# Performance work log

Hardware: AMD Instinct MI355X
Metric: run time of the kernel (lower is better)

The kernel has to match this reference:

```python
import jax, jax.numpy as jnp
import numpy as np

HIDDEN = 512
NSTEPS = 100
IN_DIM = 3
OUT_DIM = 3
BATCH = 16384


def _gru_cell(x, h, w_ih, w_hh, b_ih, b_hh):
    # torch.nn.GRUCell math; w_ih: [3H, in], w_hh: [3H, H]
    gi = x @ w_ih.T + b_ih  # [B, 3H]
    gh = h @ w_hh.T + b_hh  # [B, 3H]
    i_r, i_z, i_n = jnp.split(gi, 3, axis=-1)
    h_r, h_z, h_n = jnp.split(gh, 3, axis=-1)
    r = jax.nn.sigmoid(i_r + h_r)
    zt = jax.nn.sigmoid(i_z + h_z)
    n = jnp.tanh(i_n + r * h_n)
    return (1.0 - zt) * n + zt * h


def setup_inputs() -> dict:
    key = jax.random.key(0)
    ks = jax.random.split(key, 12)
    k = 1.0 / np.sqrt(HIDDEN)
    u = lambda kk, shape: jax.random.uniform(kk, shape, jnp.float32, -k, k)
    return {
        "z": jax.random.normal(ks[0], (BATCH, 6), jnp.float32),
        "w_ih1": u(ks[1], (3 * HIDDEN, IN_DIM)),
        "w_hh1": u(ks[2], (3 * HIDDEN, HIDDEN)),
        "b_ih1": u(ks[3], (3 * HIDDEN,)),
        "b_hh1": u(ks[4], (3 * HIDDEN,)),
        "w_ih2": u(ks[5], (3 * HIDDEN, HIDDEN)),
        "w_hh2": u(ks[6], (3 * HIDDEN, HIDDEN)),
        "b_ih2": u(ks[7], (3 * HIDDEN,)),
        "b_hh2": u(ks[8], (3 * HIDDEN,)),
        "fc_w": u(ks[9], (OUT_DIM, HIDDEN)),
        "fc_b": u(ks[10], (OUT_DIM,)),
    }


def reference(z, w_ih1, w_hh1, b_ih1, b_hh1, w_ih2, w_hh2, b_ih2, b_hh2, fc_w, fc_b):
    nbatch = z.shape[0]
    x0 = z[:, 3:]  # [B, 3]
    h1 = jnp.zeros((nbatch, HIDDEN), z.dtype)
    h2 = jnp.zeros((nbatch, HIDDEN), z.dtype)

    def step(carry, _):
        x, h1, h2 = carry
        h1 = _gru_cell(x, h1, w_ih1, w_hh1, b_ih1, b_hh1)
        h2 = _gru_cell(h1, h2, w_ih2, w_hh2, b_ih2, b_hh2)
        x = x + 0.1 * jnp.tanh(h2 @ fc_w.T + fc_b)
        return (x, h1, h2), x

    _, xs = jax.lax.scan(step, (x0, h1, h2), None, length=NSTEPS - 1)
    seq = jnp.concatenate([x0[None], xs], axis=0)  # [T, B, 3]
    return jnp.transpose(seq, (1, 0, 2))  # [B, T, 3]
```

## Files before the change

kernel.cpp:

```cpp
#include <hip/hip_runtime.h>

typedef _Float16 f16;
typedef _Float16 f16x8 __attribute__((ext_vector_type(8)));
typedef float f32x16 __attribute__((ext_vector_type(16)));
typedef unsigned int u32;
typedef u32 u32x2v __attribute__((ext_vector_type(2)));

#define HID   512
#define NSTEP 100

__device__ __forceinline__ f16x8 dec8(u32x2v w) {
  union { u32 u[4]; f16x8 v; } r;
  const u32 a = w[0], b = w[1];
  r.u[0] = ((a & 0x000000ffu) << 8) | ((a & 0x0000ff00u) << 16);
  r.u[1] = ((a >> 8) & 0x0000ff00u) | (a & 0xff000000u);
  r.u[2] = ((b & 0x000000ffu) << 8) | ((b & 0x0000ff00u) << 16);
  r.u[3] = ((b >> 8) & 0x0000ff00u) | (b & 0xff000000u);
  return r.v;
}

__device__ __forceinline__ float sigmoid_f(float x) {
  return 1.0f / (1.0f + __expf(-x));
}
__device__ __forceinline__ float tanh_f(float x) {
  float e = __expf(2.0f * x);
  return 1.0f - 2.0f / (e + 1.0f);
}
__device__ __forceinline__ f32x16 mfma16(f16x8 a, f16x8 b, f32x16 c) {
  return __builtin_amdgcn_mfma_f32_32x32x16_f16(a, b, c, 0, 0, 0);
}
__device__ __forceinline__ f32x16 zero16() {
  f32x16 z;
#pragma unroll
  for (int i = 0; i < 16; ++i) z[i] = 0.f;
  return z;
}

__global__ void pack_wn(const float* __restrict__ W, f16* __restrict__ out) {
  int t = blockIdx.x * 256 + threadIdx.x;
  if (t >= 16 * 32 * 64) return;
  int lane = t & 63;
  int kt   = (t >> 6) & 31;
  int ct   = t >> 11;
  int gate = 1024 + ct * 32 + (lane & 31);
  int k0   = kt * 16 + (lane >> 5) * 8;
  const float* src = W + gate * HID + k0;
  f16x8 v;
#pragma unroll
  for (int i = 0; i < 8; ++i) v[i] = (f16)src[i];
  *(f16x8*)(out + (size_t)t * 8) = v;
}

__global__ void pack_w8(const float* __restrict__ W, unsigned char* __restrict__ out) {
  int t = blockIdx.x * 256 + threadIdx.x;
  if (t >= 2 * 16 * 32 * 64) return;
  int lane = t & 63;
  int kt   = (t >> 6) & 31;
  int ct   = (t >> 11) & 15;
  int g    = t >> 15;
  int gate = g * 512 + ct * 32 + (lane & 31);
  int k0   = kt * 16 + (lane >> 5) * 8;
  const float* src = W + gate * HID + k0;
  unsigned char v[8];
#pragma unroll
  for (int i = 0; i < 8; ++i) {
    f16 h = (f16)src[i];
    unsigned short hb;
    __builtin_memcpy(&hb, &h, 2);
    v[i] = (unsigned char)((hb + 0x80u) >> 8);
  }
  unsigned char* dst = out + (size_t)t * 8;
#pragma unroll
  for (int i = 0; i < 8; ++i) dst[i] = v[i];
}

__global__ void pack_wx(const float* __restrict__ W, const float* __restrict__ bi,
                        const float* __restrict__ bh, f16* __restrict__ out) {
  int t = blockIdx.x * 256 + threadIdx.x;
  if (t >= 48 * 64) return;
  int lane = t & 63;
  int ct   = t >> 6;
  int col  = ct * 32 + (lane & 31);
  int k0   = (lane >> 5) * 8;
  f16x8 v;
#pragma unroll
  for (int i = 0; i < 8; ++i) {
    int k = k0 + i;
    float x = 0.f;
    if (k < 3)       x = W[col * 3 + k];
    else if (k == 3) x = (ct < 32) ? (bi[col] + bh[col]) : bi[col];
    v[i] = (f16)x;
  }
  *(f16x8*)(out + (size_t)t * 8) = v;
}

__global__ void pack_bias(const float* __restrict__ bi, const float* __restrict__ bh,
                          float* __restrict__ out) {
  int j = blockIdx.x * 256 + threadIdx.x;
  if (j < 1024)      out[j] = bi[j] + bh[j];
  else if (j < 1536) out[j] = bi[j];
  else if (j < 2048) out[j] = bh[j - 512];
}

__global__ __launch_bounds__(512, 2) void gru_fused(
    const float* __restrict__ z,
    const float* __restrict__ fc_w,
    const float* __restrict__ fc_b,
    const f16*  __restrict__ Wn,
    const unsigned char* __restrict__ W8,
    const f16*  __restrict__ Wx,
    const float* __restrict__ Bb,
    float* __restrict__ out)
{
  __shared__ f16   h1s[64 * HID];
  __shared__ f16   h2s[64 * HID];
  __shared__ f16   xs16[64 * 16];
  __shared__ float fcwT[3 * HID];
  __shared__ float xsf[64 * 4];
  __shared__ float bsh[5 * 512];

  const int tid  = threadIdx.x;
  const int lane = tid & 63;
  const int wv   = tid >> 6;
  const int b0   = blockIdx.x * 64;

  {
    f16x8 z8 = {0, 0, 0, 0, 0, 0, 0, 0};
    for (int i = tid; i < 64 * HID / 8; i += 512) {
      ((f16x8*)h1s)[i] = z8;
      ((f16x8*)h2s)[i] = z8;
    }
    if (tid < 64) {
#pragma unroll
      for (int k = 0; k < 16; ++k) xs16[tid * 16 + k] = (f16)((k == 3) ? 1.f : 0.f);
    }
    if (tid < HID) {
      const int pos = ((tid & 7) << 6) + (tid >> 3);
      fcwT[pos]        = fc_w[tid];
      fcwT[512 + pos]  = fc_w[512 + tid];
      fcwT[1024 + pos] = fc_w[1024 + tid];
      bsh[tid]         = Bb[1536 + tid];
      bsh[512 + tid]   = Bb[2048 + tid];
      bsh[1024 + tid]  = Bb[2048 + 512 + tid];
      bsh[1536 + tid]  = Bb[2048 + 1024 + tid];
      bsh[2048 + tid]  = Bb[2048 + 1536 + tid];
    }
  }
  __syncthreads();
  if (tid < 64 * 3) {
    const int rr = tid / 3, oo = tid - rr * 3;
    float v = z[(size_t)(b0 + rr) * 6 + 3 + oo];
    xsf[rr * 4 + oo] = v;
    xs16[rr * 16 + oo] = (f16)v;
    out[(size_t)(b0 + rr) * 300 + oo] = v;
  }
  __syncthreads();

  const int colid = lane & 31;
  const int khalf = lane >> 5;
  const int klo   = khalf << 4;
  const int patA  = (colid & 7) << 4;
  const int rbase = colid * 1024;
  const int jw    = wv << 6;
  const int ct0   = wv << 1;
  const int ct1   = ct0 + 1;

  const unsigned char* W8_1r = W8 + (size_t)ct0 * 16384 + lane * 8;
  const unsigned char* W8_1z = W8 + 262144 + (size_t)ct0 * 16384 + lane * 8;
  const unsigned char* W8_ir = W8 + 524288 + (size_t)ct0 * 16384 + lane * 8;
  const unsigned char* W8_iz = W8 + 524288 + 262144 + (size_t)ct0 * 16384 + lane * 8;
  const unsigned char* W8_hr = W8 + 1048576 + (size_t)ct0 * 16384 + lane * 8;
  const unsigned char* W8_hz = W8 + 1048576 + 262144 + (size_t)ct0 * 16384 + lane * 8;
  const f16* Wn_1 = Wn + (size_t)ct0 * 16384 + lane * 8;
  const f16* Wn_i = Wn + 262144 + (size_t)ct0 * 16384 + lane * 8;
  const f16* Wn_h = Wn + 524288 + (size_t)ct0 * 16384 + lane * 8;

  const float fb0 = fc_b[0], fb1 = fc_b[1], fb2 = fc_b[2];
  const int xoff0 = colid * 32 + klo;
  const int xoff1 = (32 + colid) * 32 + klo;

  for (int t = 1; t < NSTEP; ++t) {
    f32x16 aR[2][2], aH[2][2], aZ[2][2];

    {
      f16x8 ax0 = *(const f16x8*)((const char*)xs16 + xoff0);
      f16x8 ax1 = *(const f16x8*)((const char*)xs16 + xoff1);
      f32x16 zz = zero16();
#pragma unroll
      for (int c = 0; c < 2; ++c) {
        f16x8 bx = *(const f16x8*)(Wx + (size_t)(ct0 + c) * 512 + lane * 8);
        aR[c][0] = mfma16(ax0, bx, zz);
        aR[c][1] = mfma16(ax1, bx, zz);
      }
#pragma unroll 2
      for (int kt = 0; kt < 32; ++kt) {
        const int koff = ((kt << 5) | klo) ^ patA;
        f16x8 a0 = *(const f16x8*)((const char*)h1s + rbase + koff);
        f16x8 a1 = *(const f16x8*)((const char*)h1s + 32768 + rbase + koff);
        f16x8 b0 = dec8(*(const u32x2v*)(W8_1r + kt * 512));
        f16x8 b1 = dec8(*(const u32x2v*)(W8_1r + 16384 + kt * 512));
        aR[0][0] = mfma16(a0, b0, aR[0][0]);  aR[0][1] = mfma16(a1, b0, aR[0][1]);
        aR[1][0] = mfma16(a0, b1, aR[1][0]);  aR[1][1] = mfma16(a1, b1, aR[1][1]);
      }
    }
    {
      f32x16 zz = zero16();
      aH[0][0] = zz; aH[0][1] = zz; aH[1][0] = zz; aH[1][1] = zz;
#pragma unroll 2
      for (int kt = 0; kt < 32; ++kt) {
        const int koff = ((kt << 5) | klo) ^ patA;
        f16x8 a0 = *(const f16x8*)((const char*)h1s + rbase + koff);
        f16x8 a1 = *(const f16x8*)((const char*)h1s + 32768 + rbase + koff);
        f16x8 b0 = *(const f16x8*)(Wn_1 + kt * 512);
        f16x8 b1 = *(const f16x8*)(Wn_1 + 16384 + kt * 512);
        aH[0][0] = mfma16(a0, b0, aH[0][0]);  aH[0][1] = mfma16(a1, b0, aH[0][1]);
        aH[1][0] = mfma16(a0, b1, aH[1][0]);  aH[1][1] = mfma16(a1, b1, aH[1][1]);
      }
    }
    {
#pragma unroll
      for (int c = 0; c < 2; ++c) {
        const float bnh = bsh[jw + (c << 5) + colid];
#pragma unroll
        for (int tl = 0; tl < 2; ++tl)
#pragma unroll
          for (int q = 0; q < 16; ++q)
            aH[c][tl][q] = sigmoid_f(aR[c][tl][q]) * (aH[c][tl][q] + bnh);
      }
      f16x8 ax0 = *(const f16x8*)((const char*)xs16 + xoff0);
      f16x8 ax1 = *(const f16x8*)((const char*)xs16 + xoff1);
#pragma unroll
      for (int c = 0; c < 2; ++c) {
        f16x8 bx = *(const f16x8*)(Wx + (size_t)(32 + ct0 + c) * 512 + lane * 8);
        aH[c][0] = mfma16(ax0, bx, aH[c][0]);
        aH[c][1] = mfma16(ax1, bx, aH[c][1]);
      }
    }
    {
      f16x8 ax0 = *(const f16x8*)((const char*)xs16 + xoff0);
      f16x8 ax1 = *(const f16x8*)((const char*)xs16 + xoff1);
      f32x16 zz = zero16();
#pragma unroll
      for (int c = 0; c < 2; ++c) {
        f16x8 bx = *(const f16x8*)(Wx + (size_t)(16 + ct0 + c) * 512 + lane * 8);
        aZ[c][0] = mfma16(ax0, bx, zz);
        aZ[c][1] = mfma16(ax1, bx, zz);
      }
#pragma unroll 2
      for (int kt = 0; kt < 32; ++kt) {
        const int koff = ((kt << 5) | klo) ^ patA;
        f16x8 a0 = *(const f16x8*)((const char*)h1s + rbase + koff);
        f16x8 a1 = *(const f16x8*)((const char*)h1s + 32768 + rbase + koff);
        f16x8 b0 = dec8(*(const u32x2v*)(W8_1z + kt * 512));
        f16x8 b1 = dec8(*(const u32x2v*)(W8_1z + 16384 + kt * 512));
        aZ[0][0] = mfma16(a0, b0, aZ[0][0]);  aZ[0][1] = mfma16(a1, b0, aZ[0][1]);
        aZ[1][0] = mfma16(a0, b1, aZ[1][0]);  aZ[1][1] = mfma16(a1, b1, aZ[1][1]);
      }
    }
    __syncthreads();
#pragma unroll
    for (int c = 0; c < 2; ++c) {
      const int jxc = 2 * (jw + (c << 5) + colid);
#pragma unroll
      for (int tl = 0; tl < 2; ++tl)
#pragma unroll
        for (int q = 0; q < 16; ++q) {
          const int row = (q & 3) + ((q >> 2) << 3) + (khalf << 2);
          f16* hp = (f16*)((char*)h1s + tl * 32768 + row * 1024 + (jxc ^ ((row & 7) << 4)));
          float zt = sigmoid_f(aZ[c][tl][q]);
          float n  = tanh_f(aH[c][tl][q]);
          float hold = (float)*hp;
          *hp = (f16)((1.0f - zt) * n + zt * hold);
        }
    }
    __syncthreads();

    {
      f32x16 zz = zero16();
      aR[0][0] = zz; aR[0][1] = zz; aR[1][0] = zz; aR[1][1] = zz;
#pragma unroll 2
      for (int kt = 0; kt < 32; ++kt) {
        const int koff = ((kt << 5) | klo) ^ patA;
        f16x8 x0 = *(const f16x8*)((const char*)h1s + rbase + koff);
        f16x8 x1 = *(const f16x8*)((const char*)h1s + 32768 + rbase + koff);
        f16x8 y0 = *(const f16x8*)((const char*)h2s + rbase + koff);
        f16x8 y1 = *(const f16x8*)((const char*)h2s + 32768 + rbase + koff);
        f16x8 bi0 = dec8(*(const u32x2v*)(W8_ir + kt * 512));
        f16x8 bi1 = dec8(*(const u32x2v*)(W8_ir + 16384 + kt * 512));
        f16x8 bh0 = dec8(*(const u32x2v*)(W8_hr + kt * 512));
        f16x8 bh1 = dec8(*(const u32x2v*)(W8_hr + 16384 + kt * 512));
        aR[0][0] = mfma16(x0, bi0, aR[0][0]);  aR[0][0] = mfma16(y0, bh0, aR[0][0]);
        aR[0][1] = mfma16(x1, bi0, aR[0][1]);  aR[0][1] = mfma16(y1, bh0, aR[0][1]);
        aR[1][0] = mfma16(x0, bi1, aR[1][0]);  aR[1][0] = mfma16(y0, bh1, aR[1][0]);
        aR[1][1] = mfma16(x1, bi1, aR[1][1]);  aR[1][1] = mfma16(y1, bh1, aR[1][1]);
      }
    }
    {
      f32x16 zz = zero16();
      aH[0][0] = zz; aH[0][1] = zz; aH[1][0] = zz; aH[1][1] = zz;
#pragma unroll 2
      for (int kt = 0; kt < 32; ++kt) {
        const int koff = ((kt << 5) | klo) ^ patA;
        f16x8 y0 = *(const f16x8*)((const char*)h2s + rbase + koff);
        f16x8 y1 = *(const f16x8*)((const char*)h2s + 32768 + rbase + koff);
        f16x8 b0 = *(const f16x8*)(Wn_h + kt * 512);
        f16x8 b1 = *(const f16x8*)(Wn_h + 16384 + kt * 512);
        aH[0][0] = mfma16(y0, b0, aH[0][0]);  aH[0][1] = mfma16(y1, b0, aH[0][1]);
        aH[1][0] = mfma16(y0, b1, aH[1][0]);  aH[1][1] = mfma16(y1, b1, aH[1][1]);
      }
    }
#pragma unroll
    for (int c = 0; c < 2; ++c) {
      const int j = jw + (c << 5) + colid;
      const float br  = bsh[512 + j];
      const float bnh = bsh[2048 + j];
#pragma unroll
      for (int tl = 0; tl < 2; ++tl)
#pragma unroll
        for (int q = 0; q < 16; ++q)
          aH[c][tl][q] = sigmoid_f(aR[c][tl][q] + br) * (aH[c][tl][q] + bnh);
    }
    {
      f32x16 zz = zero16();
      aZ[0][0] = zz; aZ[0][1] = zz; aZ[1][0] = zz; aZ[1][1] = zz;
#pragma unroll 2
      for (int kt = 0; kt < 32; ++kt) {
        const int koff = ((kt << 5) | klo) ^ patA;
        f16x8 x0 = *(const f16x8*)((const char*)h1s + rbase + koff);
        f16x8 x1 = *(const f16x8*)((const char*)h1s + 32768 + rbase + koff);
        f16x8 y0 = *(const f16x8*)((const char*)h2s + rbase + koff);
        f16x8 y1 = *(const f16x8*)((const char*)h2s + 32768 + rbase + koff);
        f16x8 bi0 = dec8(*(const u32x2v*)(W8_iz + kt * 512));
        f16x8 bi1 = dec8(*(const u32x2v*)(W8_iz + 16384 + kt * 512));
        f16x8 bh0 = dec8(*(const u32x2v*)(W8_hz + kt * 512));
        f16x8 bh1 = dec8(*(const u32x2v*)(W8_hz + 16384 + kt * 512));
        aZ[0][0] = mfma16(x0, bi0, aZ[0][0]);  aZ[0][0] = mfma16(y0, bh0, aZ[0][0]);
        aZ[0][1] = mfma16(x1, bi0, aZ[0][1]);  aZ[0][1] = mfma16(y1, bh0, aZ[0][1]);
        aZ[1][0] = mfma16(x0, bi1, aZ[1][0]);  aZ[1][0] = mfma16(y0, bh1, aZ[1][0]);
        aZ[1][1] = mfma16(x1, bi1, aZ[1][1]);  aZ[1][1] = mfma16(y1, bh1, aZ[1][1]);
      }
    }
    {
#pragma unroll 2
      for (int kt = 0; kt < 32; ++kt) {
        const int koff = ((kt << 5) | klo) ^ patA;
        f16x8 x0 = *(const f16x8*)((const char*)h1s + rbase + koff);
        f16x8 x1 = *(const f16x8*)((const char*)h1s + 32768 + rbase + koff);
        f16x8 b0 = *(const f16x8*)(Wn_i + kt * 512);
        f16x8 b1 = *(const f16x8*)(Wn_i + 16384 + kt * 512);
        aH[0][0] = mfma16(x0, b0, aH[0][0]);  aH[0][1] = mfma16(x1, b0, aH[0][1]);
        aH[1][0] = mfma16(x0, b1, aH[1][0]);  aH[1][1] = mfma16(x1, b1, aH[1][1]);
      }
    }
    __syncthreads();
#pragma unroll
    for (int c = 0; c < 2; ++c) {
      const int j = jw + (c << 5) + colid;
      const float bz  = bsh[1024 + j];
      const float bni = bsh[1536 + j];
      const int jxc = 2 * j;
#pragma unroll
      for (int tl = 0; tl < 2; ++tl)
#pragma unroll
        for (int q = 0; q < 16; ++q) {
          const int row = (q & 3) + ((q >> 2) << 3) + (khalf << 2);
          f16* hp = (f16*)((char*)h2s + tl * 32768 + row * 1024 + (jxc ^ ((row & 7) << 4)));
          float zt = sigmoid_f(aZ[c][tl][q] + bz);
          float n  = tanh_f(aH[c][tl][q] + bni);
          float hold = (float)*hp;
          *hp = (f16)((1.0f - zt) * n + zt * hold);
        }
    }
    __syncthreads();

    {
      const int rowg = (wv << 3) + (lane >> 3);
      const int tl   = rowg >> 5;
      const int rit  = rowg & 31;
      const int sl   = lane & 7;
      const char* hb = (const char*)h2s + tl * 32768 + rit * 1024;
      const int pat = (rit & 7) << 4;
      float p0 = 0.f, p1 = 0.f, p2 = 0.f;
#pragma unroll
      for (int j = 0; j < 8; ++j) {
        f16x8 hh = *(const f16x8*)(hb + (((sl << 7) | (j << 4)) ^ pat));
#pragma unroll
        for (int i = 0; i < 8; ++i) {
          const float hf = (float)hh[i];
          const int pos = (i << 6) + (sl << 3) + j;
          p0 = fmaf(hf, fcwT[pos], p0);
          p1 = fmaf(hf, fcwT[512 + pos], p1);
          p2 = fmaf(hf, fcwT[1024 + pos], p2);
        }
      }
#pragma unroll
      for (int m = 1; m < 8; m <<= 1) {
        p0 += __shfl_xor(p0, m, 64);
        p1 += __shfl_xor(p1, m, 64);
        p2 += __shfl_xor(p2, m, 64);
      }
      if (sl == 0) {
        float x0 = xsf[(rowg << 2) + 0] + 0.1f * tanh_f(p0 + fb0);
        float x1 = xsf[(rowg << 2) + 1] + 0.1f * tanh_f(p1 + fb1);
        float x2 = xsf[(rowg << 2) + 2] + 0.1f * tanh_f(p2 + fb2);
        xsf[(rowg << 2) + 0] = x0;  xs16[rowg * 16 + 0] = (f16)x0;
        xsf[(rowg << 2) + 1] = x1;  xs16[rowg * 16 + 1] = (f16)x1;
        xsf[(rowg << 2) + 2] = x2;  xs16[rowg * 16 + 2] = (f16)x2;
        float* op = out + (size_t)(b0 + rowg) * 300 + (size_t)t * 3;
        op[0] = x0; op[1] = x1; op[2] = x2;
      }
    }
    __syncthreads();
  }
}

extern "C" void kernel_launch(void* const* d_in, const int* in_sizes, int n_in,
                              void* d_out, int out_size, void* d_ws, size_t ws_size,
                              hipStream_t stream) {
  const float* z     = (const float*)d_in[0];
  const float* w_ih1 = (const float*)d_in[1];
  const float* w_hh1 = (const float*)d_in[2];
  const float* b_ih1 = (const float*)d_in[3];
  const float* b_hh1 = (const float*)d_in[4];
  const float* w_ih2 = (const float*)d_in[5];
  const float* w_hh2 = (const float*)d_in[6];
  const float* b_ih2 = (const float*)d_in[7];
  const float* b_hh2 = (const float*)d_in[8];
  const float* fc_w  = (const float*)d_in[9];
  const float* fc_b  = (const float*)d_in[10];
  float* out = (float*)d_out;

  f16*           Wn = (f16*)d_ws;
  unsigned char* W8 = (unsigned char*)d_ws + (size_t)3 * 262144 * 2;
  f16*           Wx = (f16*)(W8 + (size_t)3 * 524288);
  float*         Bb = (float*)((char*)Wx + (size_t)48 * 512 * 2);

  const int nbatch = in_sizes[0] / 6;

  pack_wn<<<128, 256, 0, stream>>>(w_hh1, Wn);
  pack_wn<<<128, 256, 0, stream>>>(w_ih2, Wn + 262144);
  pack_wn<<<128, 256, 0, stream>>>(w_hh2, Wn + 2 * 262144);
  pack_w8<<<256, 256, 0, stream>>>(w_hh1, W8);
  pack_w8<<<256, 256, 0, stream>>>(w_ih2, W8 + 524288);
  pack_w8<<<256, 256, 0, stream>>>(w_hh2, W8 + 2 * 524288);
  pack_wx<<<12, 256, 0, stream>>>(w_ih1, b_ih1, b_hh1, Wx);
  pack_bias<<<8, 256, 0, stream>>>(b_ih1, b_hh1, Bb);
  pack_bias<<<8, 256, 0, stream>>>(b_ih2, b_hh2, Bb + 2048);

  gru_fused<<<nbatch / 64, 512, 0, stream>>>(z, fc_w, fc_b, Wn, W8, Wx, Bb, out);
}
```

Before: 11.31 ms.

## Quantize n-gate weights to 8-bit, batch-prefetch weight chunks, use perm decode

The n-gate weights, which were stored as fp16, are now also kept in the truncated 8-bit fp16-high-byte format, so every recurrent GEMM streams half as many weight bytes. Each k-loop is split into chunks whose weights are loaded into registers up front before the MFMAs run, to hide global/L2 latency. The byte-to-fp16 expansion now uses v_perm instead of shift/mask sequences. In exchange it costs accuracy on the n gate and adds register pressure from the prefetch arrays, which may spill under launch_bounds(512,2).

```diff
diff --git a/kernel.cpp b/kernel.cpp
--- a/kernel.cpp
+++ b/kernel.cpp
@@ -11,11 +11,10 @@
 
 __device__ __forceinline__ f16x8 dec8(u32x2v w) {
   union { u32 u[4]; f16x8 v; } r;
-  const u32 a = w[0], b = w[1];
-  r.u[0] = ((a & 0x000000ffu) << 8) | ((a & 0x0000ff00u) << 16);
-  r.u[1] = ((a >> 8) & 0x0000ff00u) | (a & 0xff000000u);
-  r.u[2] = ((b & 0x000000ffu) << 8) | ((b & 0x0000ff00u) << 16);
-  r.u[3] = ((b >> 8) & 0x0000ff00u) | (b & 0xff000000u);
+  r.u[0] = __builtin_amdgcn_perm(w[0], w[0], 0x010C000Cu);
+  r.u[1] = __builtin_amdgcn_perm(w[0], w[0], 0x030C020Cu);
+  r.u[2] = __builtin_amdgcn_perm(w[1], w[1], 0x010C000Cu);
+  r.u[3] = __builtin_amdgcn_perm(w[1], w[1], 0x030C020Cu);
   return r.v;
 }
 
@@ -36,24 +35,9 @@
   return z;
 }
 
-__global__ void pack_wn(const float* __restrict__ W, f16* __restrict__ out) {
-  int t = blockIdx.x * 256 + threadIdx.x;
-  if (t >= 16 * 32 * 64) return;
-  int lane = t & 63;
-  int kt   = (t >> 6) & 31;
-  int ct   = t >> 11;
-  int gate = 1024 + ct * 32 + (lane & 31);
-  int k0   = kt * 16 + (lane >> 5) * 8;
-  const float* src = W + gate * HID + k0;
-  f16x8 v;
-#pragma unroll
-  for (int i = 0; i < 8; ++i) v[i] = (f16)src[i];
-  *(f16x8*)(out + (size_t)t * 8) = v;
-}
-
 __global__ void pack_w8(const float* __restrict__ W, unsigned char* __restrict__ out) {
   int t = blockIdx.x * 256 + threadIdx.x;
-  if (t >= 2 * 16 * 32 * 64) return;
+  if (t >= 3 * 16 * 32 * 64) return;
   int lane = t & 63;
   int kt   = (t >> 6) & 31;
   int ct   = (t >> 11) & 15;
@@ -106,7 +90,6 @@
     const float* __restrict__ z,
     const float* __restrict__ fc_w,
     const float* __restrict__ fc_b,
-    const f16*  __restrict__ Wn,
     const unsigned char* __restrict__ W8,
     const f16*  __restrict__ Wx,
     const float* __restrict__ Bb,
@@ -163,17 +146,16 @@
   const int rbase = colid * 1024;
   const int jw    = wv << 6;
   const int ct0   = wv << 1;
-  const int ct1   = ct0 + 1;
 
   const unsigned char* W8_1r = W8 + (size_t)ct0 * 16384 + lane * 8;
-  const unsigned char* W8_1z = W8 + 262144 + (size_t)ct0 * 16384 + lane * 8;
-  const unsigned char* W8_ir = W8 + 524288 + (size_t)ct0 * 16384 + lane * 8;
-  const unsigned char* W8_iz = W8 + 524288 + 262144 + (size_t)ct0 * 16384 + lane * 8;
-  const unsigned char* W8_hr = W8 + 1048576 + (size_t)ct0 * 16384 + lane * 8;
-  const unsigned char* W8_hz = W8 + 1048576 + 262144 + (size_t)ct0 * 16384 + lane * 8;
-  const f16* Wn_1 = Wn + (size_t)ct0 * 16384 + lane * 8;
-  const f16* Wn_i = Wn + 262144 + (size_t)ct0 * 16384 + lane * 8;
-  const f16* Wn_h = Wn + 524288 + (size_t)ct0 * 16384 + lane * 8;
+  const unsigned char* W8_1z = W8_1r + 262144;
+  const unsigned char* W8_1n = W8_1r + 524288;
+  const unsigned char* W8_ir = W8_1r + 786432;
+  const unsigned char* W8_iz = W8_1r + 786432 + 262144;
+  const unsigned char* W8_in = W8_1r + 786432 + 524288;
+  const unsigned char* W8_hr = W8_1r + 1572864;
+  const unsigned char* W8_hz = W8_1r + 1572864 + 262144;
+  const unsigned char* W8_hn = W8_1r + 1572864 + 524288;
 
   const float fb0 = fc_b[0], fb1 = fc_b[1], fb2 = fc_b[2];
   const int xoff0 = colid * 32 + klo;
@@ -192,29 +174,51 @@
         aR[c][0] = mfma16(ax0, bx, zz);
         aR[c][1] = mfma16(ax1, bx, zz);
       }
-#pragma unroll 2
-      for (int kt = 0; kt < 32; ++kt) {
-        const int koff = ((kt << 5) | klo) ^ patA;
-        f16x8 a0 = *(const f16x8*)((const char*)h1s + rbase + koff);
-        f16x8 a1 = *(const f16x8*)((const char*)h1s + 32768 + rbase + koff);
-        f16x8 b0 = dec8(*(const u32x2v*)(W8_1r + kt * 512));
-        f16x8 b1 = dec8(*(const u32x2v*)(W8_1r + 16384 + kt * 512));
-        aR[0][0] = mfma16(a0, b0, aR[0][0]);  aR[0][1] = mfma16(a1, b0, aR[0][1]);
-        aR[1][0] = mfma16(a0, b1, aR[1][0]);  aR[1][1] = mfma16(a1, b1, aR[1][1]);
+#pragma unroll 1
+      for (int ch = 0; ch < 2; ++ch) {
+        u32x2v w0[16], w1[16];
+        const unsigned char* p = W8_1r + ch * 8192;
+#pragma unroll
+        for (int i = 0; i < 16; ++i) {
+          w0[i] = *(const u32x2v*)(p + i * 512);
+          w1[i] = *(const u32x2v*)(p + 16384 + i * 512);
+        }
+#pragma unroll
+        for (int i = 0; i < 16; ++i) {
+          const int kt = (ch << 4) + i;
+          const int koff = ((kt << 5) | klo) ^ patA;
+          f16x8 a0 = *(const f16x8*)((const char*)h1s + rbase + koff);
+          f16x8 a1 = *(const f16x8*)((const char*)h1s + 32768 + rbase + koff);
+          f16x8 b0 = dec8(w0[i]);
+          f16x8 b1 = dec8(w1[i]);
+          aR[0][0] = mfma16(a0, b0, aR[0][0]);  aR[0][1] = mfma16(a1, b0, aR[0][1]);
+          aR[1][0] = mfma16(a0, b1, aR[1][0]);  aR[1][1] = mfma16(a1, b1, aR[1][1]);
+        }
       }
     }
     {
       f32x16 zz = zero16();
       aH[0][0] = zz; aH[0][1] = zz; aH[1][0] = zz; aH[1][1] = zz;
-#pragma unroll 2
-      for (int kt = 0; kt < 32; ++kt) {
-        const int koff = ((kt << 5) | klo) ^ patA;
-        f16x8 a0 = *(const f16x8*)((const char*)h1s + rbase + koff);
-        f16x8 a1 = *(const f16x8*)((const char*)h1s + 32768 + rbase + koff);
-        f16x8 b0 = *(const f16x8*)(Wn_1 + kt * 512);
-        f16x8 b1 = *(const f16x8*)(Wn_1 + 16384 + kt * 512);
-        aH[0][0] = mfma16(a0, b0, aH[0][0]);  aH[0][1] = mfma16(a1, b0, aH[0][1]);
-        aH[1][0] = mfma16(a0, b1, aH[1][0]);  aH[1][1] = mfma16(a1, b1, aH[1][1]);
+#pragma unroll 1
+      for (int ch = 0; ch < 2; ++ch) {
+        u32x2v w0[16], w1[16];
+        const unsigned char* p = W8_1n + ch * 8192;
+#pragma unroll
+        for (int i = 0; i < 16; ++i) {
+          w0[i] = *(const u32x2v*)(p + i * 512);
+          w1[i] = *(const u32x2v*)(p + 16384 + i * 512);
+        }
+#pragma unroll
+        for (int i = 0; i < 16; ++i) {
+          const int kt = (ch << 4) + i;
+          const int koff = ((kt << 5) | klo) ^ patA;
+          f16x8 a0 = *(const f16x8*)((const char*)h1s + rbase + koff);
+          f16x8 a1 = *(const f16x8*)((const char*)h1s + 32768 + rbase + koff);
+          f16x8 b0 = dec8(w0[i]);
+          f16x8 b1 = dec8(w1[i]);
+          aH[0][0] = mfma16(a0, b0, aH[0][0]);  aH[0][1] = mfma16(a1, b0, aH[0][1]);
+          aH[1][0] = mfma16(a0, b1, aH[1][0]);  aH[1][1] = mfma16(a1, b1, aH[1][1]);
+        }
       }
     }
     {
@@ -246,15 +250,26 @@
         aZ[c][0] = mfma16(ax0, bx, zz);
         aZ[c][1] = mfma16(ax1, bx, zz);
       }
-#pragma unroll 2
-      for (int kt = 0; kt < 32; ++kt) {
-        const int koff = ((kt << 5) | klo) ^ patA;
-        f16x8 a0 = *(const f16x8*)((const char*)h1s + rbase + koff);
-        f16x8 a1 = *(const f16x8*)((const char*)h1s + 32768 + rbase + koff);
-        f16x8 b0 = dec8(*(const u32x2v*)(W8_1z + kt * 512));
-        f16x8 b1 = dec8(*(const u32x2v*)(W8_1z + 16384 + kt * 512));
-        aZ[0][0] = mfma16(a0, b0, aZ[0][0]);  aZ[0][1] = mfma16(a1, b0, aZ[0][1]);
-        aZ[1][0] = mfma16(a0, b1, aZ[1][0]);  aZ[1][1] = mfma16(a1, b1, aZ[1][1]);
+#pragma unroll 1
+      for (int ch = 0; ch < 2; ++ch) {
+        u32x2v w0[16], w1[16];
+        const unsigned char* p = W8_1z + ch * 8192;
+#pragma unroll
+        for (int i = 0; i < 16; ++i) {
+          w0[i] = *(const u32x2v*)(p + i * 512);
+          w1[i] = *(const u32x2v*)(p + 16384 + i * 512);
+        }
+#pragma unroll
+        for (int i = 0; i < 16; ++i) {
+          const int kt = (ch << 4) + i;
+          const int koff = ((kt << 5) | klo) ^ patA;
+          f16x8 a0 = *(const f16x8*)((const char*)h1s + rbase + koff);
+          f16x8 a1 = *(const f16x8*)((const char*)h1s + 32768 + rbase + koff);
+          f16x8 b0 = dec8(w0[i]);
+          f16x8 b1 = dec8(w1[i]);
+          aZ[0][0] = mfma16(a0, b0, aZ[0][0]);  aZ[0][1] = mfma16(a1, b0, aZ[0][1]);
+          aZ[1][0] = mfma16(a0, b1, aZ[1][0]);  aZ[1][1] = mfma16(a1, b1, aZ[1][1]);
+        }
       }
     }
     __syncthreads();
@@ -278,35 +293,59 @@
     {
       f32x16 zz = zero16();
       aR[0][0] = zz; aR[0][1] = zz; aR[1][0] = zz; aR[1][1] = zz;
-#pragma unroll 2
-      for (int kt = 0; kt < 32; ++kt) {
-        const int koff = ((kt << 5) | klo) ^ patA;
-        f16x8 x0 = *(const f16x8*)((const char*)h1s + rbase + koff);
-        f16x8 x1 = *(const f16x8*)((const char*)h1s + 32768 + rbase + koff);
-        f16x8 y0 = *(const f16x8*)((const char*)h2s + rbase + koff);
-        f16x8 y1 = *(const f16x8*)((const char*)h2s + 32768 + rbase + koff);
-        f16x8 bi0 = dec8(*(const u32x2v*)(W8_ir + kt * 512));
-        f16x8 bi1 = dec8(*(const u32x2v*)(W8_ir + 16384 + kt * 512));
-        f16x8 bh0 = dec8(*(const u32x2v*)(W8_hr + kt * 512));
-        f16x8 bh1 = dec8(*(const u32x2v*)(W8_hr + 16384 + kt * 512));
-        aR[0][0] = mfma16(x0, bi0, aR[0][0]);  aR[0][0] = mfma16(y0, bh0, aR[0][0]);
-        aR[0][1] = mfma16(x1, bi0, aR[0][1]);  aR[0][1] = mfma16(y1, bh0, aR[0][1]);
-        aR[1][0] = mfma16(x0, bi1, aR[1][0]);  aR[1][0] = mfma16(y0, bh1, aR[1][0]);
-        aR[1][1] = mfma16(x1, bi1, aR[1][1]);  aR[1][1] = mfma16(y1, bh1, aR[1][1]);
+#pragma unroll 1
+      for (int ch = 0; ch < 4; ++ch) {
+        u32x2v wi0[8], wi1[8], wh0[8], wh1[8];
+        const int cb = ch * 4096;
+#pragma unroll
+        for (int i = 0; i < 8; ++i) {
+          wi0[i] = *(const u32x2v*)(W8_ir + cb + i * 512);
+          wi1[i] = *(const u32x2v*)(W8_ir + 16384 + cb + i * 512);
+          wh0[i] = *(const u32x2v*)(W8_hr + cb + i * 512);
+          wh1[i] = *(const u32x2v*)(W8_hr + 16384 + cb + i * 512);
+        }
+#pragma unroll
+        for (int i = 0; i < 8; ++i) {
+          const int kt = (ch << 3) + i;
+          const int koff = ((kt << 5) | klo) ^ patA;
+          f16x8 x0 = *(const f16x8*)((const char*)h1s + rbase + koff);
+          f16x8 x1 = *(const f16x8*)((const char*)h1s + 32768 + rbase + koff);
+          f16x8 y0 = *(const f16x8*)((const char*)h2s + rbase + koff);
+          f16x8 y1 = *(const f16x8*)((const char*)h2s + 32768 + rbase + koff);
+          f16x8 bi0 = dec8(wi0[i]);
+          f16x8 bi1 = dec8(wi1[i]);
+          f16x8 bh0 = dec8(wh0[i]);
+          f16x8 bh1 = dec8(wh1[i]);
+          aR[0][0] = mfma16(x0, bi0, aR[0][0]);  aR[0][0] = mfma16(y0, bh0, aR[0][0]);
+          aR[0][1] = mfma16(x1, bi0, aR[0][1]);  aR[0][1] = mfma16(y1, bh0, aR[0][1]);
+          aR[1][0] = mfma16(x0, bi1, aR[1][0]);  aR[1][0] = mfma16(y0, bh1, aR[1][0]);
+          aR[1][1] = mfma16(x1, bi1, aR[1][1]);  aR[1][1] = mfma16(y1, bh1, aR[1][1]);
+        }
       }
     }
     {
       f32x16 zz = zero16();
       aH[0][0] = zz; aH[0][1] = zz; aH[1][0] = zz; aH[1][1] = zz;
-#pragma unroll 2
-      for (int kt = 0; kt < 32; ++kt) {
-        const int koff = ((kt << 5) | klo) ^ patA;
-        f16x8 y0 = *(const f16x8*)((const char*)h2s + rbase + koff);
-        f16x8 y1 = *(const f16x8*)((const char*)h2s + 32768 + rbase + koff);
-        f16x8 b0 = *(const f16x8*)(Wn_h + kt * 512);
-        f16x8 b1 = *(const f16x8*)(Wn_h + 16384 + kt * 512);
-        aH[0][0] = mfma16(y0, b0, aH[0][0]);  aH[0][1] = mfma16(y1, b0, aH[0][1]);
-        aH[1][0] = mfma16(y0, b1, aH[1][0]);  aH[1][1] = mfma16(y1, b1, aH[1][1]);
+#pragma unroll 1
+      for (int ch = 0; ch < 2; ++ch) {
+        u32x2v w0[16], w1[16];
+        const unsigned char* p = W8_hn + ch * 8192;
+#pragma unroll
+        for (int i = 0; i < 16; ++i) {
+          w0[i] = *(const u32x2v*)(p + i * 512);
+          w1[i] = *(const u32x2v*)(p + 16384 + i * 512);
+        }
+#pragma unroll
+        for (int i = 0; i < 16; ++i) {
+          const int kt = (ch << 4) + i;
+          const int koff = ((kt << 5) | klo) ^ patA;
+          f16x8 y0 = *(const f16x8*)((const char*)h2s + rbase + koff);
+          f16x8 y1 = *(const f16x8*)((const char*)h2s + 32768 + rbase + koff);
+          f16x8 b0 = dec8(w0[i]);
+          f16x8 b1 = dec8(w1[i]);
+          aH[0][0] = mfma16(y0, b0, aH[0][0]);  aH[0][1] = mfma16(y1, b0, aH[0][1]);
+          aH[1][0] = mfma16(y0, b1, aH[1][0]);  aH[1][1] = mfma16(y1, b1, aH[1][1]);
+        }
       }
     }
 #pragma unroll
@@ -323,33 +362,57 @@
     {
       f32x16 zz = zero16();
       aZ[0][0] = zz; aZ[0][1] = zz; aZ[1][0] = zz; aZ[1][1] = zz;
-#pragma unroll 2
-      for (int kt = 0; kt < 32; ++kt) {
-        const int koff = ((kt << 5) | klo) ^ patA;
-        f16x8 x0 = *(const f16x8*)((const char*)h1s + rbase + koff);
-        f16x8 x1 = *(const f16x8*)((const char*)h1s + 32768 + rbase + koff);
-        f16x8 y0 = *(const f16x8*)((const char*)h2s + rbase + koff);
-        f16x8 y1 = *(const f16x8*)((const char*)h2s + 32768 + rbase + koff);
-        f16x8 bi0 = dec8(*(const u32x2v*)(W8_iz + kt * 512));
-        f16x8 bi1 = dec8(*(const u32x2v*)(W8_iz + 16384 + kt * 512));
-        f16x8 bh0 = dec8(*(const u32x2v*)(W8_hz + kt * 512));
-        f16x8 bh1 = dec8(*(const u32x2v*)(W8_hz + 16384 + kt * 512));
-        aZ[0][0] = mfma16(x0, bi0, aZ[0][0]);  aZ[0][0] = mfma16(y0, bh0, aZ[0][0]);
-        aZ[0][1] = mfma16(x1, bi0, aZ[0][1]);  aZ[0][1] = mfma16(y1, bh0, aZ[0][1]);
-        aZ[1][0] = mfma16(x0, bi1, aZ[1][0]);  aZ[1][0] = mfma16(y0, bh1, aZ[1][0]);
-        aZ[1][1] = mfma16(x1, bi1, aZ[1][1]);  aZ[1][1] = mfma16(y1, bh1, aZ[1][1]);
-      }
-    }
-    {
-#pragma unroll 2
-      for (int kt = 0; kt < 32; ++kt) {
-        const int koff = ((kt << 5) | klo) ^ patA;
-        f16x8 x0 = *(const f16x8*)((const char*)h1s + rbase + koff);
-        f16x8 x1 = *(const f16x8*)((const char*)h1s + 32768 + rbase + koff);
-        f16x8 b0 = *(const f16x8*)(Wn_i + kt * 512);
-        f16x8 b1 = *(const f16x8*)(Wn_i + 16384 + kt * 512);
-        aH[0][0] = mfma16(x0, b0, aH[0][0]);  aH[0][1] = mfma16(x1, b0, aH[0][1]);
-        aH[1][0] = mfma16(x0, b1, aH[1][0]);  aH[1][1] = mfma16(x1, b1, aH[1][1]);
+#pragma unroll 1
+      for (int ch = 0; ch < 4; ++ch) {
+        u32x2v wi0[8], wi1[8], wh0[8], wh1[8];
+        const int cb = ch * 4096;
+#pragma unroll
+        for (int i = 0; i < 8; ++i) {
+          wi0[i] = *(const u32x2v*)(W8_iz + cb + i * 512);
+          wi1[i] = *(const u32x2v*)(W8_iz + 16384 + cb + i * 512);
+          wh0[i] = *(const u32x2v*)(W8_hz + cb + i * 512);
+          wh1[i] = *(const u32x2v*)(W8_hz + 16384 + cb + i * 512);
+        }
+#pragma unroll
+        for (int i = 0; i < 8; ++i) {
+          const int kt = (ch << 3) + i;
+          const int koff = ((kt << 5) | klo) ^ patA;
+          f16x8 x0 = *(const f16x8*)((const char*)h1s + rbase + koff);
+          f16x8 x1 = *(const f16x8*)((const char*)h1s + 32768 + rbase + koff);
+          f16x8 y0 = *(const f16x8*)((const char*)h2s + rbase + koff);
+          f16x8 y1 = *(const f16x8*)((const char*)h2s + 32768 + rbase + koff);
+          f16x8 bi0 = dec8(wi0[i]);
+          f16x8 bi1 = dec8(wi1[i]);
+          f16x8 bh0 = dec8(wh0[i]);
+          f16x8 bh1 = dec8(wh1[i]);
+          aZ[0][0] = mfma16(x0, bi0, aZ[0][0]);  aZ[0][0] = mfma16(y0, bh0, aZ[0][0]);
+          aZ[0][1] = mfma16(x1, bi0, aZ[0][1]);  aZ[0][1] = mfma16(y1, bh0, aZ[0][1]);
+          aZ[1][0] = mfma16(x0, bi1, aZ[1][0]);  aZ[1][0] = mfma16(y0, bh1, aZ[1][0]);
+          aZ[1][1] = mfma16(x1, bi1, aZ[1][1]);  aZ[1][1] = mfma16(y1, bh1, aZ[1][1]);
+        }
+      }
+    }
+    {
+#pragma unroll 1
+      for (int ch = 0; ch < 2; ++ch) {
+        u32x2v w0[16], w1[16];
+        const unsigned char* p = W8_in + ch * 8192;
+#pragma unroll
+        for (int i = 0; i < 16; ++i) {
+          w0[i] = *(const u32x2v*)(p + i * 512);
+          w1[i] = *(const u32x2v*)(p + 16384 + i * 512);
+        }
+#pragma unroll
+        for (int i = 0; i < 16; ++i) {
+          const int kt = (ch << 4) + i;
+          const int koff = ((kt << 5) | klo) ^ patA;
+          f16x8 x0 = *(const f16x8*)((const char*)h1s + rbase + koff);
+          f16x8 x1 = *(const f16x8*)((const char*)h1s + 32768 + rbase + koff);
+          f16x8 b0 = dec8(w0[i]);
+          f16x8 b1 = dec8(w1[i]);
+          aH[0][0] = mfma16(x0, b0, aH[0][0]);  aH[0][1] = mfma16(x1, b0, aH[0][1]);
+          aH[1][0] = mfma16(x0, b1, aH[1][0]);  aH[1][1] = mfma16(x1, b1, aH[1][1]);
+        }
       }
     }
     __syncthreads();
@@ -430,22 +493,18 @@
   const float* fc_b  = (const float*)d_in[10];
   float* out = (float*)d_out;
 
-  f16*           Wn = (f16*)d_ws;
-  unsigned char* W8 = (unsigned char*)d_ws + (size_t)3 * 262144 * 2;
-  f16*           Wx = (f16*)(W8 + (size_t)3 * 524288);
+  unsigned char* W8 = (unsigned char*)d_ws;
+  f16*           Wx = (f16*)(W8 + (size_t)3 * 786432);
   float*         Bb = (float*)((char*)Wx + (size_t)48 * 512 * 2);
 
   const int nbatch = in_sizes[0] / 6;
 
-  pack_wn<<<128, 256, 0, stream>>>(w_hh1, Wn);
-  pack_wn<<<128, 256, 0, stream>>>(w_ih2, Wn + 262144);
-  pack_wn<<<128, 256, 0, stream>>>(w_hh2, Wn + 2 * 262144);
-  pack_w8<<<256, 256, 0, stream>>>(w_hh1, W8);
-  pack_w8<<<256, 256, 0, stream>>>(w_ih2, W8 + 524288);
-  pack_w8<<<256, 256, 0, stream>>>(w_hh2, W8 + 2 * 524288);
+  pack_w8<<<384, 256, 0, stream>>>(w_hh1, W8);
+  pack_w8<<<384, 256, 0, stream>>>(w_ih2, W8 + 786432);
+  pack_w8<<<384, 256, 0, stream>>>(w_hh2, W8 + 2 * 786432);
   pack_wx<<<12, 256, 0, stream>>>(w_ih1, b_ih1, b_hh1, Wx);
   pack_bias<<<8, 256, 0, stream>>>(b_ih1, b_hh1, Bb);
   pack_bias<<<8, 256, 0, stream>>>(b_ih2, b_hh2, Bb + 2048);
 
-  gru_fused<<<nbatch / 64, 512, 0, stream>>>(z, fc_w, fc_b, Wn, W8, Wx, Bb, out);
-}
+  gru_fused<<<nbatch / 64, 512, 0, stream>>>(z, fc_w, fc_b, W8, Wx, Bb, out);
+}
```

Result: slower. 12.81 ms (+13.3%).
